# Kernel optimization log

Measured on AMD Instinct MI355X. Metric: run time of the kernel, lower is better.

The kernel has to match this reference:

```python
import jax, jax.numpy as jnp
import numpy as np

TEMPERATURE = 0.05
EPS = 1e-8  # matches torch F.cosine_similarity eps default


def setup_inputs() -> dict:
    key = jax.random.key(0)
    k1, k2 = jax.random.split(key)
    N, D = 8192, 512
    query_embeddings = jax.random.normal(k1, (N, D), dtype=jnp.float32)
    pos_embeddings = jax.random.normal(k2, (N, D), dtype=jnp.float32)
    return {"query_embeddings": query_embeddings, "pos_embeddings": pos_embeddings}


def reference(query_embeddings, pos_embeddings):
    # cosine_similarity(q[:,None,:], p[None,:,:], dim=2) == normalize(q) @ normalize(p).T
    qn = query_embeddings / jnp.maximum(
        jnp.linalg.norm(query_embeddings, axis=-1, keepdims=True), EPS)
    pn = pos_embeddings / jnp.maximum(
        jnp.linalg.norm(pos_embeddings, axis=-1, keepdims=True), EPS)
    sim = jnp.einsum('nd,md->nm', qn, pn) / TEMPERATURE  # [N, N] logits
    # cross-entropy with targets = arange(N): diagonal logits are the positives
    logz = jax.nn.logsumexp(sim, axis=-1)               # [N]
    diag = jnp.diagonal(sim)                             # [N]
    loss = jnp.mean(logz - diag)
    return loss
```

## Files before the change

### kernel.cpp

```cpp
#include <hip/hip_runtime.h>
#include <hip/hip_bf16.h>

#define NROWS 8192
#define DIM 512
#define BM 256
#define BN 256

typedef int   i32x4 __attribute__((ext_vector_type(4)));
typedef int   i32x8 __attribute__((ext_vector_type(8)));
typedef float f32x4 __attribute__((ext_vector_type(4)));

#define FP8_SCALE_1 0x7f7f7f7f

__global__ __launch_bounds__(128) void prep_k(
    const float* __restrict__ q, const float* __restrict__ p,
    char* __restrict__ qf, char* __restrict__ pf,
    float* __restrict__ diag) {
  const int i = blockIdx.x;
  const int t = threadIdx.x;
  const int lane = t & 63, wid = t >> 6;
  const float4 qv = ((const float4*)(q + (size_t)i * DIM))[t];
  const float4 pv = ((const float4*)(p + (size_t)i * DIM))[t];
  float ssq = qv.x*qv.x + qv.y*qv.y + qv.z*qv.z + qv.w*qv.w;
  float ssp = pv.x*pv.x + pv.y*pv.y + pv.z*pv.z + pv.w*pv.w;
  float dt  = qv.x*pv.x + qv.y*pv.y + qv.z*pv.z + qv.w*pv.w;
  #pragma unroll
  for (int m = 1; m < 64; m <<= 1) {
    ssq += __shfl_xor(ssq, m, 64);
    ssp += __shfl_xor(ssp, m, 64);
    dt  += __shfl_xor(dt,  m, 64);
  }
  __shared__ float red[3][2];
  if (lane == 0) { red[0][wid] = ssq; red[1][wid] = ssp; red[2][wid] = dt; }
  __syncthreads();
  ssq = red[0][0] + red[0][1];
  ssp = red[1][0] + red[1][1];
  dt  = red[2][0] + red[2][1];
  const float invq = 1.0f / fmaxf(sqrtf(ssq), 1e-8f);
  const float invp = 1.0f / fmaxf(sqrtf(ssp), 1e-8f);
  int rq = 0, rp = 0;
  rq = __builtin_amdgcn_cvt_pk_fp8_f32(qv.x * invq, qv.y * invq, rq, false);
  rq = __builtin_amdgcn_cvt_pk_fp8_f32(qv.z * invq, qv.w * invq, rq, true);
  rp = __builtin_amdgcn_cvt_pk_fp8_f32(pv.x * invp, pv.y * invp, rp, false);
  rp = __builtin_amdgcn_cvt_pk_fp8_f32(pv.z * invp, pv.w * invp, rp, true);

  const int panel = i >> 8, lr = i & 255;
  const int kt  = t >> 5;
  const int l4g = (t >> 3) & 3;
  const int sel = (t >> 2) & 1;
  const int byo = (t & 3) * 4;
  const int laneT = l4g * 16 + (lr & 15);
  const size_t addrA =
      ((((size_t)(panel * 4 + kt) * 2 + (lr >> 7)) * 8 + ((lr >> 4) & 7)) * 2 + sel) * 1024
      + laneT * 16 + byo;
  const size_t addrB =
      ((((size_t)(panel * 4 + kt) * 4 + (lr >> 6)) * 4 + ((lr >> 4) & 3)) * 2 + sel) * 1024
      + laneT * 16 + byo;
  *(unsigned int*)(qf + addrA) = (unsigned int)rq;
  *(unsigned int*)(pf + addrB) = (unsigned int)rp;
  if (t == 0) diag[i] = dt * invq * invp * 20.0f;
}

__global__ __launch_bounds__(512, 2) void gemm_lse_k(
    const char* __restrict__ qf, const char* __restrict__ pf,
    float* __restrict__ partial) {
  __shared__ float psum[1024];
  const int tid = threadIdx.x;
  const int lane = tid & 63, wid = tid >> 6;
  const int wr = wid >> 2, wc = wid & 3;
  const int l15 = lane & 15, l4 = lane >> 4;
  const int b = blockIdx.x;
  const int g = b & 7;
  const int j = b >> 3;
  const int panelA = (g & 3) * 8 + (j & 7);
  const int bnset  = (g >> 2) * 16 + (j >> 3) * 4;
  const int bm = panelA * BM;
  const char* aPanel = qf + (size_t)panelA * 131072 + (size_t)lane * 16;
  const char* pBase  = pf + (size_t)lane * 16;

  f32x4 acc[4][8] = {};
  i32x8 af[8], bf[4];

  #pragma unroll 1
  for (int tt = 0; tt < 16; ++tt) {
    const int kt = tt & 3, t = tt >> 2;
    const char* aB = aPanel + (size_t)(kt * 2 + wr) * 16384;
    const char* bB = pBase +
        (size_t)(((bnset + t) * 4 + kt) * 4 + wc) * 8192;

    #pragma unroll
    for (int mf = 0; mf < 8; ++mf) {
      const i32x4 lo = *(const i32x4*)(aB + mf * 2048);
      const i32x4 hi = *(const i32x4*)(aB + mf * 2048 + 1024);
      af[mf] = __builtin_shufflevector(lo, hi, 0, 1, 2, 3, 4, 5, 6, 7);
    }
    #pragma unroll
    for (int nf = 0; nf < 4; ++nf) {
      const i32x4 lo = *(const i32x4*)(bB + nf * 2048);
      const i32x4 hi = *(const i32x4*)(bB + nf * 2048 + 1024);
      bf[nf] = __builtin_shufflevector(lo, hi, 0, 1, 2, 3, 4, 5, 6, 7);
    }

    __builtin_amdgcn_s_setprio(1);
    #pragma unroll
    for (int nb = 0; nb < 4; ++nb)
      #pragma unroll
      for (int am = 0; am < 8; ++am)
        acc[nb][am] = __builtin_amdgcn_mfma_scale_f32_16x16x128_f8f6f4(
            bf[nb], af[am], acc[nb][am], 0, 0, 0, FP8_SCALE_1, 0, FP8_SCALE_1);
    __builtin_amdgcn_s_setprio(0);

    if ((tt & 3) == 3) {
      const int bxc = bnset + t;
      #pragma unroll
      for (int am = 0; am < 8; ++am) {
        float s = 0.0f;
        #pragma unroll
        for (int nb = 0; nb < 4; ++nb)
          #pragma unroll
          for (int r = 0; r < 4; ++r)
            s += __expf(acc[nb][am][r] * 20.0f - 20.0f);
        s += __shfl_xor(s, 16, 64);
        s += __shfl_xor(s, 32, 64);
        if (l4 == 0)
          psum[wc * 256 + wr * 128 + am * 16 + l15] = s;
      }
      __syncthreads();
      if (tid < 256)
        partial[(size_t)(bm + tid) * 32 + bxc] =
            psum[tid] + psum[256 + tid] + psum[512 + tid] + psum[768 + tid];
      __syncthreads();
      #pragma unroll
      for (int nb = 0; nb < 4; ++nb)
        #pragma unroll
        for (int am = 0; am < 8; ++am)
          acc[nb][am] = f32x4{0.0f, 0.0f, 0.0f, 0.0f};
    }
  }
}

__global__ __launch_bounds__(256) void rowloss_k(
    const float* __restrict__ partial, const float* __restrict__ diag,
    float* __restrict__ rowloss) {
  const int i = blockIdx.x * 256 + threadIdx.x;
  const float4* pr = (const float4*)(partial + (size_t)i * 32);
  float s = 0.0f;
  #pragma unroll
  for (int c = 0; c < 8; ++c) {
    const float4 v = pr[c];
    s += v.x + v.y + v.z + v.w;
  }
  rowloss[i] = __logf(s) + 20.0f - diag[i];
}

__global__ __launch_bounds__(1024) void final_k(
    const float* __restrict__ rowloss, float* __restrict__ out) {
  const int t = threadIdx.x;
  float s = 0.0f;
  #pragma unroll
  for (int j = 0; j < 8; ++j) s += rowloss[t + j * 1024];
  #pragma unroll
  for (int m = 1; m < 64; m <<= 1) s += __shfl_xor(s, m, 64);
  __shared__ float red[16];
  if ((t & 63) == 0) red[t >> 6] = s;
  __syncthreads();
  if (t == 0) {
    float acc = 0.0f;
    #pragma unroll
    for (int w = 0; w < 16; ++w) acc += red[w];
    out[0] = acc * (1.0f / (float)NROWS);
  }
}

extern "C" void kernel_launch(void* const* d_in, const int* in_sizes, int n_in,
                              void* d_out, int out_size, void* d_ws, size_t ws_size,
                              hipStream_t stream) {
  const float* q = (const float*)d_in[0];
  const float* p = (const float*)d_in[1];
  char* w = (char*)d_ws;
  char* qf = w;
  char* pf = w + 4194304;
  float* partial    = (float*)(w + 8388608);
  float* diag       = (float*)(w + 9437184);
  float* rowloss    = (float*)(w + 9437184 + 32768);
  float* out = (float*)d_out;

  prep_k<<<NROWS, 128, 0, stream>>>(q, p, qf, pf, diag);
  gemm_lse_k<<<256, 512, 0, stream>>>(qf, pf, partial);
  rowloss_k<<<NROWS / 256, 256, 0, stream>>>(partial, diag, rowloss);
  final_k<<<1, 1024, 0, stream>>>(rowloss, out);
}
```

Baseline: 62.76 us.

## Coalesce prep writes via LDS staging and double the GEMM grid

The prep kernel now handles 16 rows per 256-thread block. It converts rows to FP8 into padded LDS, then writes contiguous 16-byte chunks into the MFMA-tiled layout instead of scattered 4-byte stores. The GEMM+LSE kernel launches 512 blocks, each covering 2 column tiles instead of 4. This lets two blocks share a CU under the existing launch bounds, improving latency hiding. The cost is more A-panel reloads across blocks and extra LDS and sync in prep.

```diff
diff --git a/kernel.cpp b/kernel.cpp
--- a/kernel.cpp
+++ b/kernel.cpp
@@ -12,53 +12,70 @@
 
 #define FP8_SCALE_1 0x7f7f7f7f
 
-__global__ __launch_bounds__(128) void prep_k(
+__global__ __launch_bounds__(256) void prep_k(
     const float* __restrict__ q, const float* __restrict__ p,
     char* __restrict__ qf, char* __restrict__ pf,
     float* __restrict__ diag) {
-  const int i = blockIdx.x;
-  const int t = threadIdx.x;
-  const int lane = t & 63, wid = t >> 6;
-  const float4 qv = ((const float4*)(q + (size_t)i * DIM))[t];
-  const float4 pv = ((const float4*)(p + (size_t)i * DIM))[t];
-  float ssq = qv.x*qv.x + qv.y*qv.y + qv.z*qv.z + qv.w*qv.w;
-  float ssp = pv.x*pv.x + pv.y*pv.y + pv.z*pv.z + pv.w*pv.w;
-  float dt  = qv.x*pv.x + qv.y*pv.y + qv.z*pv.z + qv.w*pv.w;
-  #pragma unroll
-  for (int m = 1; m < 64; m <<= 1) {
+  __shared__ char ldsq[16 * 528];
+  __shared__ char ldsp[16 * 528];
+  const int tid = threadIdx.x;
+  const int blk = blockIdx.x;
+  const int rr = tid >> 4;
+  const int cs = tid & 15;
+  const int i  = blk * 16 + rr;
+  const float4* qr = (const float4*)(q + (size_t)i * DIM);
+  const float4* pr = (const float4*)(p + (size_t)i * DIM);
+
+  float4 qv[8], pv[8];
+  float ssq = 0.0f, ssp = 0.0f, dt = 0.0f;
+  #pragma unroll
+  for (int jj = 0; jj < 8; ++jj) {
+    qv[jj] = qr[jj * 16 + cs];
+    pv[jj] = pr[jj * 16 + cs];
+    ssq += qv[jj].x*qv[jj].x + qv[jj].y*qv[jj].y + qv[jj].z*qv[jj].z + qv[jj].w*qv[jj].w;
+    ssp += pv[jj].x*pv[jj].x + pv[jj].y*pv[jj].y + pv[jj].z*pv[jj].z + pv[jj].w*pv[jj].w;
+    dt  += qv[jj].x*pv[jj].x + qv[jj].y*pv[jj].y + qv[jj].z*pv[jj].z + qv[jj].w*pv[jj].w;
+  }
+  #pragma unroll
+  for (int m = 1; m < 16; m <<= 1) {
     ssq += __shfl_xor(ssq, m, 64);
     ssp += __shfl_xor(ssp, m, 64);
     dt  += __shfl_xor(dt,  m, 64);
   }
-  __shared__ float red[3][2];
-  if (lane == 0) { red[0][wid] = ssq; red[1][wid] = ssp; red[2][wid] = dt; }
-  __syncthreads();
-  ssq = red[0][0] + red[0][1];
-  ssp = red[1][0] + red[1][1];
-  dt  = red[2][0] + red[2][1];
   const float invq = 1.0f / fmaxf(sqrtf(ssq), 1e-8f);
   const float invp = 1.0f / fmaxf(sqrtf(ssp), 1e-8f);
-  int rq = 0, rp = 0;
-  rq = __builtin_amdgcn_cvt_pk_fp8_f32(qv.x * invq, qv.y * invq, rq, false);
-  rq = __builtin_amdgcn_cvt_pk_fp8_f32(qv.z * invq, qv.w * invq, rq, true);
-  rp = __builtin_amdgcn_cvt_pk_fp8_f32(pv.x * invp, pv.y * invp, rp, false);
-  rp = __builtin_amdgcn_cvt_pk_fp8_f32(pv.z * invp, pv.w * invp, rp, true);
-
-  const int panel = i >> 8, lr = i & 255;
-  const int kt  = t >> 5;
-  const int l4g = (t >> 3) & 3;
-  const int sel = (t >> 2) & 1;
-  const int byo = (t & 3) * 4;
-  const int laneT = l4g * 16 + (lr & 15);
-  const size_t addrA =
-      ((((size_t)(panel * 4 + kt) * 2 + (lr >> 7)) * 8 + ((lr >> 4) & 7)) * 2 + sel) * 1024
-      + laneT * 16 + byo;
-  const size_t addrB =
-      ((((size_t)(panel * 4 + kt) * 4 + (lr >> 6)) * 4 + ((lr >> 4) & 3)) * 2 + sel) * 1024
-      + laneT * 16 + byo;
-  *(unsigned int*)(qf + addrA) = (unsigned int)rq;
-  *(unsigned int*)(pf + addrB) = (unsigned int)rp;
-  if (t == 0) diag[i] = dt * invq * invp * 20.0f;
+  if (cs == 0) diag[i] = dt * invq * invp * 20.0f;
+
+  #pragma unroll
+  for (int jj = 0; jj < 8; ++jj) {
+    int rq = 0, rp = 0;
+    rq = __builtin_amdgcn_cvt_pk_fp8_f32(qv[jj].x * invq, qv[jj].y * invq, rq, false);
+    rq = __builtin_amdgcn_cvt_pk_fp8_f32(qv[jj].z * invq, qv[jj].w * invq, rq, true);
+    rp = __builtin_amdgcn_cvt_pk_fp8_f32(pv[jj].x * invp, pv[jj].y * invp, rp, false);
+    rp = __builtin_amdgcn_cvt_pk_fp8_f32(pv[jj].z * invp, pv[jj].w * invp, rp, true);
+    *(unsigned int*)(ldsq + rr * 528 + jj * 64 + cs * 4) = (unsigned int)rq;
+    *(unsigned int*)(ldsp + rr * 528 + jj * 64 + cs * 4) = (unsigned int)rp;
+  }
+  __syncthreads();
+
+  const int panel = blk >> 4, rg = blk & 15;
+  #pragma unroll
+  for (int u = 0; u < 2; ++u) {
+    const int o = 2 * tid + u;
+    const int kt = o >> 7, sel = (o >> 6) & 1, laneT = o & 63;
+    const int rrs = laneT & 15;
+    const int srcoff = kt * 128 + (laneT >> 4) * 32 + sel * 16;
+    const i32x4 va = *(const i32x4*)(ldsq + rrs * 528 + srcoff);
+    const size_t aaddr =
+        ((((size_t)(panel * 4 + kt) * 2 + (rg >> 3)) * 8 + (rg & 7)) * 2 + sel) * 1024
+        + laneT * 16;
+    *(i32x4*)(qf + aaddr) = va;
+    const i32x4 vb = *(const i32x4*)(ldsp + rrs * 528 + srcoff);
+    const size_t baddr =
+        ((((size_t)(panel * 4 + kt) * 4 + (rg >> 2)) * 4 + (rg & 3)) * 2 + sel) * 1024
+        + laneT * 16;
+    *(i32x4*)(pf + baddr) = vb;
+  }
 }
 
 __global__ __launch_bounds__(512, 2) void gemm_lse_k(
@@ -73,7 +90,7 @@
   const int g = b & 7;
   const int j = b >> 3;
   const int panelA = (g & 3) * 8 + (j & 7);
-  const int bnset  = (g >> 2) * 16 + (j >> 3) * 4;
+  const int bnset  = (g >> 2) * 16 + (j >> 3) * 2;
   const int bm = panelA * BM;
   const char* aPanel = qf + (size_t)panelA * 131072 + (size_t)lane * 16;
   const char* pBase  = pf + (size_t)lane * 16;
@@ -82,7 +99,7 @@
   i32x8 af[8], bf[4];
 
   #pragma unroll 1
-  for (int tt = 0; tt < 16; ++tt) {
+  for (int tt = 0; tt < 8; ++tt) {
     const int kt = tt & 3, t = tt >> 2;
     const char* aB = aPanel + (size_t)(kt * 2 + wr) * 16384;
     const char* bB = pBase +
@@ -185,8 +202,8 @@
   float* rowloss    = (float*)(w + 9437184 + 32768);
   float* out = (float*)d_out;
 
-  prep_k<<<NROWS, 128, 0, stream>>>(q, p, qf, pf, diag);
-  gemm_lse_k<<<256, 512, 0, stream>>>(qf, pf, partial);
+  prep_k<<<NROWS / 16, 256, 0, stream>>>(q, p, qf, pf, diag);
+  gemm_lse_k<<<512, 512, 0, stream>>>(qf, pf, partial);
   rowloss_k<<<NROWS / 256, 256, 0, stream>>>(partial, diag, rowloss);
   final_k<<<1, 1024, 0, stream>>>(rowloss, out);
 }
```

Measured after the change: 58.18 us. -7.3%, faster.
